# Performance work log

Measured on AMD Instinct MI355X. Metric: run time of the kernel, lower is better.

Reference implementation:

```python
import jax, jax.numpy as jnp
import numpy as np

D_MODEL = 512
NHEAD = 8
D_K = D_MODEL // NHEAD
SCALE = float(np.sqrt(D_K))


def setup_inputs() -> dict:
    key = jax.random.key(0)
    ks = jax.random.split(key, 11)
    B, S = 2, 4096
    std = 1.0 / np.sqrt(D_MODEL)
    inp = {
        'q': jax.random.normal(ks[0], (B, S, D_MODEL), jnp.float32),
        'k': jax.random.normal(ks[1], (B, S, D_MODEL), jnp.float32),
        'v': jax.random.normal(ks[2], (B, S, D_MODEL), jnp.float32),
        'w_q': jax.random.normal(ks[3], (D_MODEL, D_MODEL), jnp.float32) * std,
        'b_q': jax.random.normal(ks[4], (D_MODEL,), jnp.float32) * std,
        'w_k': jax.random.normal(ks[5], (D_MODEL, D_MODEL), jnp.float32) * std,
        'b_k': jax.random.normal(ks[6], (D_MODEL,), jnp.float32) * std,
        'w_v': jax.random.normal(ks[7], (D_MODEL, D_MODEL), jnp.float32) * std,
        'b_v': jax.random.normal(ks[8], (D_MODEL,), jnp.float32) * std,
        'w_o': jax.random.normal(ks[9], (D_MODEL, D_MODEL), jnp.float32) * std,
        'b_o': jax.random.normal(ks[10], (D_MODEL,), jnp.float32) * std,
    }
    return inp


def reference(q, k, v, w_q, b_q, w_k, b_k, w_v, b_v, w_o, b_o):
    B, S, _ = q.shape
    # torch Linear: y = x @ W.T + b
    def proj(x, W, b):
        y = x @ W.T + b
        return y.reshape(B, -1, NHEAD, D_K).transpose(0, 2, 1, 3)  # [B,H,S,Dk]
    qh = proj(q, w_q, b_q)
    kh = proj(k, w_k, b_k)
    vh = proj(v, w_v, b_v)
    scores = jnp.einsum('bhsd,bhtd->bhst', qh, kh) / SCALE  # [B,H,S,S]
    attn = jax.nn.softmax(scores, axis=-1)
    out = jnp.einsum('bhst,bhtd->bhsd', attn, vh)  # [B,H,S,Dk]
    out = out.transpose(0, 2, 1, 3).reshape(B, S, D_MODEL)
    return out @ w_o.T + b_o
```

## Files before the change

### kernel.cpp

```cpp
#include <hip/hip_runtime.h>
#include <stdint.h>

#define DM 512
#define S_LEN 4096
#define NH 8
#define DK 64

typedef __attribute__((ext_vector_type(8))) short bf16x8;
typedef __attribute__((ext_vector_type(4))) float f32x4;

#define QSCALE 0.18033688011112042f
#define NEGBIAS -17.312340490667562f

__device__ inline ushort f2bf(float f) {
  union { float f; uint32_t u; } v; v.f = f;
  uint32_t r = v.u + 0x7fff + ((v.u >> 16) & 1);
  return (ushort)(r >> 16);
}
__device__ inline uint32_t fu(float f) {
  union { float f; uint32_t u; } v; v.f = f; return v.u;
}
__device__ inline uint32_t pktrunc(float lo, float hi) {
  return __builtin_amdgcn_perm(fu(hi), fu(lo), 0x07060302);
}

__device__ inline void async_cp16(const ushort* g, ushort* l) {
  __builtin_amdgcn_global_load_lds((const __attribute__((address_space(1))) void*)g,
                                   (__attribute__((address_space(3))) void*)l, 16, 0, 0);
}

__global__ __launch_bounds__(256) void cvt_all(
    const float4* __restrict__ s0, ushort* __restrict__ d0,
    const float4* __restrict__ s1, ushort* __restrict__ d1,
    const float4* __restrict__ s2, ushort* __restrict__ d2,
    const float4* __restrict__ s3, ushort* __restrict__ d3,
    const float4* __restrict__ x0, ushort* __restrict__ y0,
    const float4* __restrict__ x1, ushort* __restrict__ y1,
    const float4* __restrict__ x2, ushort* __restrict__ y2) {
  if (blockIdx.x < 256) {
    int i = blockIdx.x * 256 + threadIdx.x;
    { float4 v = s0[i]; ushort4 o = {f2bf(v.x), f2bf(v.y), f2bf(v.z), f2bf(v.w)}; *(ushort4*)&d0[i * 4] = o; }
    { float4 v = s1[i]; ushort4 o = {f2bf(v.x), f2bf(v.y), f2bf(v.z), f2bf(v.w)}; *(ushort4*)&d1[i * 4] = o; }
    { float4 v = s2[i]; ushort4 o = {f2bf(v.x), f2bf(v.y), f2bf(v.z), f2bf(v.w)}; *(ushort4*)&d2[i * 4] = o; }
    { float4 v = s3[i]; ushort4 o = {f2bf(v.x), f2bf(v.y), f2bf(v.z), f2bf(v.w)}; *(ushort4*)&d3[i * 4] = o; }
  } else {
    int b = blockIdx.x - 256;
    #pragma unroll
    for (int r = 0; r < 2; r++) {
      int i = (b * 2 + r) * 256 + threadIdx.x;
      { float4 v = x0[i]; ushort4 o = {f2bf(v.x), f2bf(v.y), f2bf(v.z), f2bf(v.w)}; *(ushort4*)&y0[i * 4] = o; }
      { float4 v = x1[i]; ushort4 o = {f2bf(v.x), f2bf(v.y), f2bf(v.z), f2bf(v.w)}; *(ushort4*)&y1[i * 4] = o; }
      { float4 v = x2[i]; ushort4 o = {f2bf(v.x), f2bf(v.y), f2bf(v.z), f2bf(v.w)}; *(ushort4*)&y2[i * 4] = o; }
    }
  }
}

__global__ __launch_bounds__(256) void gemm_proj(
    const ushort* __restrict__ xq, const ushort* __restrict__ xk, const ushort* __restrict__ xv,
    const ushort* __restrict__ wq, const ushort* __restrict__ wk, const ushort* __restrict__ wv,
    const float* __restrict__ bq, const float* __restrict__ bk, const float* __restrict__ bv,
    ushort* __restrict__ Qh, ushort* __restrict__ Kh, ushort* __restrict__ VhT) {
  const ushort* A; const ushort* Bt; const float* bias; float cs;
  if (blockIdx.z == 0)      { A = xq; Bt = wq; bias = bq; cs = QSCALE; }
  else if (blockIdx.z == 1) { A = xk; Bt = wk; bias = bk; cs = 1.0f; }
  else                      { A = xv; Bt = wv; bias = bv; cs = 1.0f; }

  __shared__ ushort As[2][64 * 32];
  __shared__ ushort Bs[2][128 * 32];
  const int tid = threadIdx.x;
  const int w = tid >> 6, lane = tid & 63;
  const int quad = lane >> 4, l16 = lane & 15;
  const int wm = w >> 1, wn = w & 1;
  const int m0 = blockIdx.x * 64, n0 = blockIdx.y * 128;
  const f32x4 zero4 = {0.f, 0.f, 0.f, 0.f};

  f32x4 acc[2][4];
  #pragma unroll
  for (int i = 0; i < 2; i++)
    #pragma unroll
    for (int j = 0; j < 4; j++) acc[i][j] = zero4;

  #define PSTAGE(KB, BUF) do {                                                        \
    const int k0_ = (KB) * 32;                                                        \
    { int idx = tid;                                                \
      async_cp16(&A[(size_t)(m0 + (idx >> 2)) * DM + k0_ + (idx & 3) * 8], &As[BUF][idx * 8]); } \
    _Pragma("unroll")                                                                 \
    for (int r_ = 0; r_ < 2; r_++) {                                \
      int idx = r_ * 256 + tid;                                                       \
      async_cp16(&Bt[(size_t)(n0 + (idx >> 2)) * DM + k0_ + (idx & 3) * 8], &Bs[BUF][idx * 8]); \
    }                                                                                 \
  } while (0)

  PSTAGE(0, 0);
  __syncthreads();

  for (int kb = 0; kb < 16; kb++) {
    const int cur = kb & 1;
    if (kb < 15) PSTAGE(kb + 1, cur ^ 1);
    bf16x8 af[2], bfr[4];
    #pragma unroll
    for (int i = 0; i < 2; i++)
      af[i]  = *(const bf16x8*)&As[cur][(wm * 32 + i * 16 + l16) * 32 + quad * 8];
    #pragma unroll
    for (int j = 0; j < 4; j++)
      bfr[j] = *(const bf16x8*)&Bs[cur][(wn * 64 + j * 16 + l16) * 32 + quad * 8];
    #pragma unroll
    for (int i = 0; i < 2; i++)
      #pragma unroll
      for (int j = 0; j < 4; j++)
        acc[i][j] = __builtin_amdgcn_mfma_f32_16x16x32_bf16(af[i], bfr[j], acc[i][j], 0, 0, 0);
    __syncthreads();
  }

  if (blockIdx.z != 2) {
    ushort* C = (blockIdx.z == 0) ? Qh : Kh;
    #pragma unroll
    for (int j = 0; j < 4; j++) {
      int col_g = n0 + wn * 64 + j * 16 + l16;
      float bv = bias[col_g];
      int h = col_g >> 6, d = col_g & 63;
      #pragma unroll
      for (int i = 0; i < 2; i++) {
        #pragma unroll
        for (int r = 0; r < 4; r++) {
          int row_g = m0 + wm * 32 + i * 16 + quad * 4 + r;
          int b = row_g >> 12, s = row_g & 4095;
          C[(((size_t)(b * NH + h) << 12) + s) * DK + d] = f2bf((acc[i][j][r] + bv) * cs);
        }
      }
    }
  } else {
    #pragma unroll
    for (int j = 0; j < 4; j++) {
      int col_g = n0 + wn * 64 + j * 16 + l16;
      float bv = bias[col_g];
      int h = col_g >> 6, d = col_g & 63;
      #pragma unroll
      for (int i = 0; i < 2; i++) {
        int row0 = m0 + wm * 32 + i * 16 + quad * 4;
        int b = row0 >> 12, s0 = row0 & 4095;
        int sl = s0 & 31;
        int sp = (s0 & ~31) | (((sl >> 2) & 3) << 3) | (((sl >> 4) & 1) << 2);
        ushort4 pk = {f2bf(acc[i][j][0] + bv), f2bf(acc[i][j][1] + bv),
                      f2bf(acc[i][j][2] + bv), f2bf(acc[i][j][3] + bv)};
        *(ushort4*)&VhT[((size_t)(b * NH + h) * DK + d) * S_LEN + sp] = pk;
      }
    }
  }
}

__global__ __launch_bounds__(256) void gemm_out(const ushort* __restrict__ A,
                                                const ushort* __restrict__ Bt,
                                                const float* __restrict__ bias,
                                                float* __restrict__ C) {
  __shared__ ushort As[2][64 * 32];
  __shared__ ushort Bs[2][128 * 32];
  const int tid = threadIdx.x;
  const int w = tid >> 6, lane = tid & 63;
  const int quad = lane >> 4, l16 = lane & 15;
  const int wm = w >> 1, wn = w & 1;
  const int m0 = blockIdx.x * 64, n0 = blockIdx.y * 128;
  const f32x4 zero4 = {0.f, 0.f, 0.f, 0.f};

  f32x4 acc[2][4];
  #pragma unroll
  for (int i = 0; i < 2; i++)
    #pragma unroll
    for (int j = 0; j < 4; j++) acc[i][j] = zero4;

  #define OSTAGE(KB, BUF) do {                                                        \
    const int k0_ = (KB) * 32;                                                        \
    { int idx = tid;                                                                  \
      async_cp16(&A[(size_t)(m0 + (idx >> 2)) * DM + k0_ + (idx & 3) * 8], &As[BUF][idx * 8]); } \
    _Pragma("unroll")                                                                 \
    for (int r_ = 0; r_ < 2; r_++) {                                                  \
      int idx = r_ * 256 + tid;                                                       \
      async_cp16(&Bt[(size_t)(n0 + (idx >> 2)) * DM + k0_ + (idx & 3) * 8], &Bs[BUF][idx * 8]); \
    }                                                                                 \
  } while (0)

  OSTAGE(0, 0);
  __syncthreads();

  for (int kb = 0; kb < 16; kb++) {
    const int cur = kb & 1;
    if (kb < 15) OSTAGE(kb + 1, cur ^ 1);
    bf16x8 af[2], bfr[4];
    #pragma unroll
    for (int i = 0; i < 2; i++)
      af[i]  = *(const bf16x8*)&As[cur][(wm * 32 + i * 16 + l16) * 32 + quad * 8];
    #pragma unroll
    for (int j = 0; j < 4; j++)
      bfr[j] = *(const bf16x8*)&Bs[cur][(wn * 64 + j * 16 + l16) * 32 + quad * 8];
    #pragma unroll
    for (int i = 0; i < 2; i++)
      #pragma unroll
      for (int j = 0; j < 4; j++)
        acc[i][j] = __builtin_amdgcn_mfma_f32_16x16x32_bf16(af[i], bfr[j], acc[i][j], 0, 0, 0);
    __syncthreads();
  }

  #pragma unroll
  for (int j = 0; j < 4; j++) {
    int col_g = n0 + wn * 64 + j * 16 + l16;
    float bv = bias[col_g];
    #pragma unroll
    for (int i = 0; i < 2; i++) {
      #pragma unroll
      for (int r = 0; r < 4; r++) {
        int row_g = m0 + wm * 32 + i * 16 + quad * 4 + r;
        C[(size_t)row_g * DM + col_g] = acc[i][j][r] + bv;
      }
    }
  }
}

typedef union { bf16x8 v; uint32_t u[4]; } pfu;

__global__ __launch_bounds__(512, 4) void attn(const ushort* __restrict__ Qh,
                                               const ushort* __restrict__ Kh,
                                               const ushort* __restrict__ VhT,
                                               ushort* __restrict__ O) {
  __shared__ ushort smem[2][16384];
  const int tid = threadIdx.x;
  const int w = tid >> 6, lane = tid & 63;
  const int quad = lane >> 4, l16 = lane & 15;
  const int half = w >> 2;
  const int qw = w & 3;
  const int bh = blockIdx.x;
  const int q0 = blockIdx.y * 128 + qw * 32;
  const size_t base = (size_t)bh * S_LEN * DK;
  const f32x4 zero4 = {0.f, 0.f, 0.f, 0.f};
  const f32x4 negb = {NEGBIAS, NEGBIAS, NEGBIAS, NEGBIAS};
  const short one_bf = (short)0x3F80;
  const bf16x8 ones = {one_bf, one_bf, one_bf, one_bf, one_bf, one_bf, one_bf, one_bf};

  if (blockIdx.y >= 16) {
    #pragma unroll
    for (int i = 0; i < 6; i++) __builtin_amdgcn_s_sleep(7);
  }

  bf16x8 qf[2][2];
  #pragma unroll
  for (int i = 0; i < 2; i++)
    #pragma unroll
    for (int c = 0; c < 2; c++)
      qf[i][c] = *(const bf16x8*)&Qh[base + (size_t)(q0 + i * 16 + l16) * DK + c * 32 + quad * 8];

  f32x4 o[2][4];
  f32x4 l_acc[2];
  #pragma unroll
  for (int i = 0; i < 2; i++) {
    l_acc[i] = zero4;
    #pragma unroll
    for (int n = 0; n < 4; n++) o[i][n] = zero4;
  }

  #define STAGE(IT, BUF) do {                                                         \
    const int t0_ = (IT) * 128;                                                       \
    _Pragma("unroll")                                                                 \
    for (int r_ = 0; r_ < 2; r_++) {                                                  \
      int idx = r_ * 512 + tid;                                                       \
      int row = idx >> 3;                                                             \
      int cl = ((idx & 7) << 4) ^ ((row & 7) << 4);                                   \
      async_cp16(&Kh[base + (size_t)(t0_ + row) * DK + (cl >> 1)], &smem[BUF][idx * 8]); \
    }                                                                                 \
    _Pragma("unroll")                                                                 \
    for (int r_ = 0; r_ < 2; r_++) {                                                  \
      int idx = r_ * 512 + tid;                                                       \
      int row = idx >> 4;                                                             \
      int cl = ((idx & 15) << 4) ^ ((row & 7) << 4);                                  \
      async_cp16(&VhT[base + (size_t)row * S_LEN + t0_ + (cl >> 1)], &smem[BUF][8192 + idx * 8]); \
    }                                                                                 \
  } while (0)

  STAGE(0, 0);
  __syncthreads();

  const int swz = (l16 & 7) << 4;

  for (int it = 0; it < 32; it++) {
    const int cur = it & 1;
    if (it < 31) STAGE(it + 1, cur ^ 1);
    const ushort* Kb = &smem[cur][0];
    const ushort* Vb = &smem[cur][8192];

    bf16x8 kf[4][2];
    #pragma unroll
    for (int s = 0; s < 4; s++) {
      int row = half * 64 + s * 16 + l16;
      kf[s][0] = *(const bf16x8*)&Kb[row * 64 + ((( 0 + quad * 16) ^ swz) >> 1)];
      kf[s][1] = *(const bf16x8*)&Kb[row * 64 + (((64 + quad * 16) ^ swz) >> 1)];
    }
    f32x4 sc[2][4];
    __builtin_amdgcn_s_setprio(1);
    #pragma unroll
    for (int i = 0; i < 2; i++)
      #pragma unroll
      for (int s = 0; s < 4; s++) {
        f32x4 t = negb;
        t = __builtin_amdgcn_mfma_f32_16x16x32_bf16(kf[s][0], qf[i][0], t, 0, 0, 0);
        t = __builtin_amdgcn_mfma_f32_16x16x32_bf16(kf[s][1], qf[i][1], t, 0, 0, 0);
        sc[i][s] = t;
      }
    __builtin_amdgcn_s_setprio(0);
    float p[2][4][4];
    #pragma unroll
    for (int i = 0; i < 2; i++)
      #pragma unroll
      for (int s = 0; s < 4; s++)
        #pragma unroll
        for (int r = 0; r < 4; r++)
          p[i][s][r] = __builtin_amdgcn_exp2f(sc[i][s][r]);
    pfu pf[2][2];
    #pragma unroll
    for (int i = 0; i < 2; i++)
      #pragma unroll
      for (int ppl = 0; ppl < 2; ppl++) {
        int s0 = ppl * 2, s1 = ppl * 2 + 1;
        pf[i][ppl].u[0] = pktrunc(p[i][s0][0], p[i][s0][1]);
        pf[i][ppl].u[1] = pktrunc(p[i][s0][2], p[i][s0][3]);
        pf[i][ppl].u[2] = pktrunc(p[i][s1][0], p[i][s1][1]);
        pf[i][ppl].u[3] = pktrunc(p[i][s1][2], p[i][s1][3]);
        l_acc[i] = __builtin_amdgcn_mfma_f32_16x16x32_bf16(pf[i][ppl].v, ones, l_acc[i], 0, 0, 0);
      }
    bf16x8 vf[4][2];
    #pragma unroll
    for (int n = 0; n < 4; n++) {
      int row = n * 16 + l16;
      #pragma unroll
      for (int ppl = 0; ppl < 2; ppl++)
        vf[n][ppl] = *(const bf16x8*)&Vb[row * 128 + ((((half * 2 + ppl) * 64 + quad * 16) ^ swz) >> 1)];
    }
    __builtin_amdgcn_s_setprio(1);
    #pragma unroll
    for (int n = 0; n < 4; n++)
      #pragma unroll
      for (int ppl = 0; ppl < 2; ppl++)
        #pragma unroll
        for (int i = 0; i < 2; i++)
          o[i][n] = __builtin_amdgcn_mfma_f32_16x16x32_bf16(pf[i][ppl].v, vf[n][ppl], o[i][n], 0, 0, 0);
    __builtin_amdgcn_s_setprio(0);

    __syncthreads();
  }

  float* red = (float*)smem;
  const int roff = (qw * 64 + lane) * 40;
  if (half == 1) {
    #pragma unroll
    for (int i = 0; i < 2; i++) {
      #pragma unroll
      for (int n = 0; n < 4; n++)
        *(f32x4*)&red[roff + (i * 4 + n) * 4] = o[i][n];
      *(f32x4*)&red[roff + 32 + i * 4] = l_acc[i];
    }
  }
  __syncthreads();
  if (half == 0) {
    #pragma unroll
    for (int i = 0; i < 2; i++) {
      #pragma unroll
      for (int n = 0; n < 4; n++)
        o[i][n] += *(const f32x4*)&red[roff + (i * 4 + n) * 4];
      l_acc[i] += *(const f32x4*)&red[roff + 32 + i * 4];
    }
    const int b = bh >> 3, h = bh & 7;
    #pragma unroll
    for (int i = 0; i < 2; i++) {
      #pragma unroll
      for (int r = 0; r < 4; r++) {
        float inv = 1.0f / l_acc[i][r];
        int qq = q0 + i * 16 + quad * 4 + r;
        #pragma unroll
        for (int n = 0; n < 4; n++) {
          int d = n * 16 + l16;
          O[(size_t)(b * S_LEN + qq) * DM + h * DK + d] = f2bf(o[i][n][r] * inv);
        }
      }
    }
  }
}

extern "C" void kernel_launch(void* const* d_in, const int* in_sizes, int n_in,
                              void* d_out, int out_size, void* d_ws, size_t ws_size,
                              hipStream_t stream) {
  const float* q   = (const float*)d_in[0];
  const float* k   = (const float*)d_in[1];
  const float* v   = (const float*)d_in[2];
  const float* w_q = (const float*)d_in[3];
  const float* b_q = (const float*)d_in[4];
  const float* w_k = (const float*)d_in[5];
  const float* b_k = (const float*)d_in[6];
  const float* w_v = (const float*)d_in[7];
  const float* b_v = (const float*)d_in[8];
  const float* w_o = (const float*)d_in[9];
  const float* b_o = (const float*)d_in[10];

  const size_t W_ELEMS = (size_t)DM * DM;
  const size_t X_ELEMS = (size_t)2 * S_LEN * DM;
  const size_t HEADS_ELEMS = (size_t)2 * NH * S_LEN * DK;
  ushort* wqb = (ushort*)d_ws;
  ushort* wkb = wqb + W_ELEMS;
  ushort* wvb = wkb + W_ELEMS;
  ushort* wob = wvb + W_ELEMS;
  ushort* Xq  = wob + W_ELEMS;
  ushort* Xk  = Xq + X_ELEMS;
  ushort* Xv  = Xk + X_ELEMS;
  ushort* Qh  = Xv + X_ELEMS;
  ushort* Kh  = Qh + HEADS_ELEMS;
  ushort* VhT = Kh + HEADS_ELEMS;
  ushort* AttO = VhT + HEADS_ELEMS;

  cvt_all<<<2304, 256, 0, stream>>>((const float4*)w_q, wqb, (const float4*)w_k, wkb,
                                    (const float4*)w_v, wvb, (const float4*)w_o, wob,
                                    (const float4*)q, Xq, (const float4*)k, Xk,
                                    (const float4*)v, Xv);
  gemm_proj<<<dim3(128, 4, 3), 256, 0, stream>>>(Xq, Xk, Xv, wqb, wkb, wvb,
                                                 b_q, b_k, b_v, Qh, Kh, VhT);
  attn<<<dim3(16, 32), 512, 0, stream>>>(Qh, Kh, VhT, AttO);
  gemm_out<<<dim3(128, 4), 256, 0, stream>>>(AttO, wob, b_o, (float*)d_out);
}
```

Measured before the change: 212.7 us.

## Fuse activation fp32-to-bf16 conversion into projection GEMM staging

Drops the separate conversion pass over the q/k/v activations. The projection GEMM now async-copies fp32 activation tiles straight into LDS and converts them to bf16 by truncation while building MFMA fragments. LDS layouts for both GEMMs are also reorganised into k-chunk-major order so each lane's fragment read is contiguous and less bank-conflicted. In exchange, the projection kernel reads twice as many activation bytes per tile, uses more LDS, and rounds by truncation instead of round-to-nearest.

```diff
diff --git a/kernel.cpp b/kernel.cpp
--- a/kernel.cpp
+++ b/kernel.cpp
@@ -24,49 +24,34 @@
   return __builtin_amdgcn_perm(fu(hi), fu(lo), 0x07060302);
 }
 
-__device__ inline void async_cp16(const ushort* g, ushort* l) {
+__device__ inline void async_cp16(const void* g, void* l) {
   __builtin_amdgcn_global_load_lds((const __attribute__((address_space(1))) void*)g,
                                    (__attribute__((address_space(3))) void*)l, 16, 0, 0);
 }
 
-__global__ __launch_bounds__(256) void cvt_all(
-    const float4* __restrict__ s0, ushort* __restrict__ d0,
-    const float4* __restrict__ s1, ushort* __restrict__ d1,
-    const float4* __restrict__ s2, ushort* __restrict__ d2,
-    const float4* __restrict__ s3, ushort* __restrict__ d3,
-    const float4* __restrict__ x0, ushort* __restrict__ y0,
-    const float4* __restrict__ x1, ushort* __restrict__ y1,
-    const float4* __restrict__ x2, ushort* __restrict__ y2) {
-  if (blockIdx.x < 256) {
-    int i = blockIdx.x * 256 + threadIdx.x;
-    { float4 v = s0[i]; ushort4 o = {f2bf(v.x), f2bf(v.y), f2bf(v.z), f2bf(v.w)}; *(ushort4*)&d0[i * 4] = o; }
-    { float4 v = s1[i]; ushort4 o = {f2bf(v.x), f2bf(v.y), f2bf(v.z), f2bf(v.w)}; *(ushort4*)&d1[i * 4] = o; }
-    { float4 v = s2[i]; ushort4 o = {f2bf(v.x), f2bf(v.y), f2bf(v.z), f2bf(v.w)}; *(ushort4*)&d2[i * 4] = o; }
-    { float4 v = s3[i]; ushort4 o = {f2bf(v.x), f2bf(v.y), f2bf(v.z), f2bf(v.w)}; *(ushort4*)&d3[i * 4] = o; }
-  } else {
-    int b = blockIdx.x - 256;
-    #pragma unroll
-    for (int r = 0; r < 2; r++) {
-      int i = (b * 2 + r) * 256 + threadIdx.x;
-      { float4 v = x0[i]; ushort4 o = {f2bf(v.x), f2bf(v.y), f2bf(v.z), f2bf(v.w)}; *(ushort4*)&y0[i * 4] = o; }
-      { float4 v = x1[i]; ushort4 o = {f2bf(v.x), f2bf(v.y), f2bf(v.z), f2bf(v.w)}; *(ushort4*)&y1[i * 4] = o; }
-      { float4 v = x2[i]; ushort4 o = {f2bf(v.x), f2bf(v.y), f2bf(v.z), f2bf(v.w)}; *(ushort4*)&y2[i * 4] = o; }
-    }
-  }
+__global__ __launch_bounds__(256) void cvt_w(const float4* __restrict__ s0, ushort* __restrict__ d0,
+                                             const float4* __restrict__ s1, ushort* __restrict__ d1,
+                                             const float4* __restrict__ s2, ushort* __restrict__ d2,
+                                             const float4* __restrict__ s3, ushort* __restrict__ d3) {
+  int i = blockIdx.x * 256 + threadIdx.x;
+  { float4 v = s0[i]; ushort4 o = {f2bf(v.x), f2bf(v.y), f2bf(v.z), f2bf(v.w)}; *(ushort4*)&d0[i * 4] = o; }
+  { float4 v = s1[i]; ushort4 o = {f2bf(v.x), f2bf(v.y), f2bf(v.z), f2bf(v.w)}; *(ushort4*)&d1[i * 4] = o; }
+  { float4 v = s2[i]; ushort4 o = {f2bf(v.x), f2bf(v.y), f2bf(v.z), f2bf(v.w)}; *(ushort4*)&d2[i * 4] = o; }
+  { float4 v = s3[i]; ushort4 o = {f2bf(v.x), f2bf(v.y), f2bf(v.z), f2bf(v.w)}; *(ushort4*)&d3[i * 4] = o; }
 }
 
 __global__ __launch_bounds__(256) void gemm_proj(
-    const ushort* __restrict__ xq, const ushort* __restrict__ xk, const ushort* __restrict__ xv,
+    const float* __restrict__ q, const float* __restrict__ k, const float* __restrict__ v,
     const ushort* __restrict__ wq, const ushort* __restrict__ wk, const ushort* __restrict__ wv,
     const float* __restrict__ bq, const float* __restrict__ bk, const float* __restrict__ bv,
     ushort* __restrict__ Qh, ushort* __restrict__ Kh, ushort* __restrict__ VhT) {
-  const ushort* A; const ushort* Bt; const float* bias; float cs;
-  if (blockIdx.z == 0)      { A = xq; Bt = wq; bias = bq; cs = QSCALE; }
-  else if (blockIdx.z == 1) { A = xk; Bt = wk; bias = bk; cs = 1.0f; }
-  else                      { A = xv; Bt = wv; bias = bv; cs = 1.0f; }
-
-  __shared__ ushort As[2][64 * 32];
-  __shared__ ushort Bs[2][128 * 32];
+  const float* A; const ushort* Bt; const float* bias; float cs;
+  if (blockIdx.z == 0)      { A = q; Bt = wq; bias = bq; cs = QSCALE; }
+  else if (blockIdx.z == 1) { A = k; Bt = wk; bias = bk; cs = 1.0f; }
+  else                      { A = v; Bt = wv; bias = bv; cs = 1.0f; }
+
+  __shared__ float  Asf[2][2048];
+  __shared__ ushort Bsp[2][4096];
   const int tid = threadIdx.x;
   const int w = tid >> 6, lane = tid & 63;
   const int quad = lane >> 4, l16 = lane & 15;
@@ -82,12 +67,17 @@
 
   #define PSTAGE(KB, BUF) do {                                                        \
     const int k0_ = (KB) * 32;                                                        \
-    { int idx = tid;                                                \
-      async_cp16(&A[(size_t)(m0 + (idx >> 2)) * DM + k0_ + (idx & 3) * 8], &As[BUF][idx * 8]); } \
     _Pragma("unroll")                                                                 \
-    for (int r_ = 0; r_ < 2; r_++) {                                \
+    for (int r_ = 0; r_ < 2; r_++) {                       \
       int idx = r_ * 256 + tid;                                                       \
-      async_cp16(&Bt[(size_t)(n0 + (idx >> 2)) * DM + k0_ + (idx & 3) * 8], &Bs[BUF][idx * 8]); \
+      int c = idx >> 6, row = idx & 63;                                               \
+      async_cp16(&A[(size_t)(m0 + row) * DM + k0_ + c * 4], &Asf[BUF][idx * 4]);      \
+    }                                                                                 \
+    _Pragma("unroll")                                                                 \
+    for (int r_ = 0; r_ < 2; r_++) {                       \
+      int idx = r_ * 256 + tid;                                                       \
+      int c = idx >> 7, row = idx & 127;                                              \
+      async_cp16(&Bt[(size_t)(n0 + row) * DM + k0_ + c * 8], &Bsp[BUF][idx * 8]);     \
     }                                                                                 \
   } while (0)
 
@@ -99,11 +89,18 @@
     if (kb < 15) PSTAGE(kb + 1, cur ^ 1);
     bf16x8 af[2], bfr[4];
     #pragma unroll
-    for (int i = 0; i < 2; i++)
-      af[i]  = *(const bf16x8*)&As[cur][(wm * 32 + i * 16 + l16) * 32 + quad * 8];
+    for (int i = 0; i < 2; i++) {
+      int r = wm * 32 + i * 16 + l16;
+      f32x4 a0 = *(const f32x4*)&Asf[cur][((quad * 2 + 0) * 64 + r) * 4];
+      f32x4 a1 = *(const f32x4*)&Asf[cur][((quad * 2 + 1) * 64 + r) * 4];
+      union { bf16x8 v; uint32_t u[4]; } t;
+      t.u[0] = pktrunc(a0.x, a0.y); t.u[1] = pktrunc(a0.z, a0.w);
+      t.u[2] = pktrunc(a1.x, a1.y); t.u[3] = pktrunc(a1.z, a1.w);
+      af[i] = t.v;
+    }
     #pragma unroll
     for (int j = 0; j < 4; j++)
-      bfr[j] = *(const bf16x8*)&Bs[cur][(wn * 64 + j * 16 + l16) * 32 + quad * 8];
+      bfr[j] = *(const bf16x8*)&Bsp[cur][(quad * 128 + wn * 64 + j * 16 + l16) * 8];
     #pragma unroll
     for (int i = 0; i < 2; i++)
       #pragma unroll
@@ -153,8 +150,8 @@
                                                 const ushort* __restrict__ Bt,
                                                 const float* __restrict__ bias,
                                                 float* __restrict__ C) {
-  __shared__ ushort As[2][64 * 32];
-  __shared__ ushort Bs[2][128 * 32];
+  __shared__ ushort Asp[2][2048];
+  __shared__ ushort Bsp[2][4096];
   const int tid = threadIdx.x;
   const int w = tid >> 6, lane = tid & 63;
   const int quad = lane >> 4, l16 = lane & 15;
@@ -170,12 +167,14 @@
 
   #define OSTAGE(KB, BUF) do {                                                        \
     const int k0_ = (KB) * 32;                                                        \
-    { int idx = tid;                                                                  \
-      async_cp16(&A[(size_t)(m0 + (idx >> 2)) * DM + k0_ + (idx & 3) * 8], &As[BUF][idx * 8]); } \
+    { int idx = tid;                                                \
+      int c = idx >> 6, row = idx & 63;                                               \
+      async_cp16(&A[(size_t)(m0 + row) * DM + k0_ + c * 8], &Asp[BUF][idx * 8]); }    \
     _Pragma("unroll")                                                                 \
-    for (int r_ = 0; r_ < 2; r_++) {                                                  \
+    for (int r_ = 0; r_ < 2; r_++) {                                \
       int idx = r_ * 256 + tid;                                                       \
-      async_cp16(&Bt[(size_t)(n0 + (idx >> 2)) * DM + k0_ + (idx & 3) * 8], &Bs[BUF][idx * 8]); \
+      int c = idx >> 7, row = idx & 127;                                              \
+      async_cp16(&Bt[(size_t)(n0 + row) * DM + k0_ + c * 8], &Bsp[BUF][idx * 8]);     \
     }                                                                                 \
   } while (0)
 
@@ -188,10 +187,10 @@
     bf16x8 af[2], bfr[4];
     #pragma unroll
     for (int i = 0; i < 2; i++)
-      af[i]  = *(const bf16x8*)&As[cur][(wm * 32 + i * 16 + l16) * 32 + quad * 8];
+      af[i]  = *(const bf16x8*)&Asp[cur][(quad * 64 + wm * 32 + i * 16 + l16) * 8];
     #pragma unroll
     for (int j = 0; j < 4; j++)
-      bfr[j] = *(const bf16x8*)&Bs[cur][(wn * 64 + j * 16 + l16) * 32 + quad * 8];
+      bfr[j] = *(const bf16x8*)&Bsp[cur][(quad * 128 + wn * 64 + j * 16 + l16) * 8];
     #pragma unroll
     for (int i = 0; i < 2; i++)
       #pragma unroll
@@ -398,25 +397,19 @@
   const float* b_o = (const float*)d_in[10];
 
   const size_t W_ELEMS = (size_t)DM * DM;
-  const size_t X_ELEMS = (size_t)2 * S_LEN * DM;
   const size_t HEADS_ELEMS = (size_t)2 * NH * S_LEN * DK;
   ushort* wqb = (ushort*)d_ws;
   ushort* wkb = wqb + W_ELEMS;
   ushort* wvb = wkb + W_ELEMS;
   ushort* wob = wvb + W_ELEMS;
-  ushort* Xq  = wob + W_ELEMS;
-  ushort* Xk  = Xq + X_ELEMS;
-  ushort* Xv  = Xk + X_ELEMS;
-  ushort* Qh  = Xv + X_ELEMS;
+  ushort* Qh  = wob + W_ELEMS;
   ushort* Kh  = Qh + HEADS_ELEMS;
   ushort* VhT = Kh + HEADS_ELEMS;
   ushort* AttO = VhT + HEADS_ELEMS;
 
-  cvt_all<<<2304, 256, 0, stream>>>((const float4*)w_q, wqb, (const float4*)w_k, wkb,
-                                    (const float4*)w_v, wvb, (const float4*)w_o, wob,
-                                    (const float4*)q, Xq, (const float4*)k, Xk,
-                                    (const float4*)v, Xv);
-  gemm_proj<<<dim3(128, 4, 3), 256, 0, stream>>>(Xq, Xk, Xv, wqb, wkb, wvb,
+  cvt_w<<<256, 256, 0, stream>>>((const float4*)w_q, wqb, (const float4*)w_k, wkb,
+                                 (const float4*)w_v, wvb, (const float4*)w_o, wob);
+  gemm_proj<<<dim3(128, 4, 3), 256, 0, stream>>>(q, k, v, wqb, wkb, wvb,
                                                  b_q, b_k, b_v, Qh, Kh, VhT);
   attn<<<dim3(16, 32), 512, 0, stream>>>(Qh, Kh, VhT, AttO);
   gemm_out<<<dim3(128, 4), 256, 0, stream>>>(AttO, wob, b_o, (float*)d_out);
```

Result: slower. 245.4 us (+15.4%).

## Triple-buffer projection GEMMs with explicit vmcnt waits and k-chunk-major LDS layout

Applied to the files above, without the earlier changes.

Both projection GEMM kernels move from a double-buffered LDS pipeline to a three-stage ring that prefetches two k-blocks ahead. A single barrier per iteration is gated by an explicit s_waitcnt vmcnt, replacing the two __syncthreads per step. The LDS tile layout changes from row-major 32-wide rows to k-chunk-major 8-element slabs, so each quad's 16-byte fragment reads fall in contiguous, bank-friendly addresses. This costs 50% more LDS per block, which may reduce occupancy, and relies on hand-counted vmcnt values that must match the number of async loads per stage.

```diff
diff --git a/kernel.cpp b/kernel.cpp
--- a/kernel.cpp
+++ b/kernel.cpp
@@ -24,7 +24,7 @@
   return __builtin_amdgcn_perm(fu(hi), fu(lo), 0x07060302);
 }
 
-__device__ inline void async_cp16(const ushort* g, ushort* l) {
+__device__ inline void async_cp16(const void* g, void* l) {
   __builtin_amdgcn_global_load_lds((const __attribute__((address_space(1))) void*)g,
                                    (__attribute__((address_space(3))) void*)l, 16, 0, 0);
 }
@@ -65,8 +65,8 @@
   else if (blockIdx.z == 1) { A = xk; Bt = wk; bias = bk; cs = 1.0f; }
   else                      { A = xv; Bt = wv; bias = bv; cs = 1.0f; }
 
-  __shared__ ushort As[2][64 * 32];
-  __shared__ ushort Bs[2][128 * 32];
+  __shared__ ushort Asp[3][2048];
+  __shared__ ushort Bsp[3][4096];
   const int tid = threadIdx.x;
   const int w = tid >> 6, lane = tid & 63;
   const int quad = lane >> 4, l16 = lane & 15;
@@ -82,34 +82,42 @@
 
   #define PSTAGE(KB, BUF) do {                                                        \
     const int k0_ = (KB) * 32;                                                        \
+    ushort* asp_ = &Asp[BUF][0];                                                      \
+    ushort* bsp_ = &Bsp[BUF][0];                                                      \
     { int idx = tid;                                                \
-      async_cp16(&A[(size_t)(m0 + (idx >> 2)) * DM + k0_ + (idx & 3) * 8], &As[BUF][idx * 8]); } \
+      int c = idx >> 6, row = idx & 63;                                               \
+      async_cp16(&A[(size_t)(m0 + row) * DM + k0_ + c * 8], &asp_[idx * 8]); }        \
     _Pragma("unroll")                                                                 \
     for (int r_ = 0; r_ < 2; r_++) {                                \
       int idx = r_ * 256 + tid;                                                       \
-      async_cp16(&Bt[(size_t)(n0 + (idx >> 2)) * DM + k0_ + (idx & 3) * 8], &Bs[BUF][idx * 8]); \
+      int c = idx >> 7, row = idx & 127;                                              \
+      async_cp16(&Bt[(size_t)(n0 + row) * DM + k0_ + c * 8], &bsp_[idx * 8]);         \
     }                                                                                 \
   } while (0)
 
   PSTAGE(0, 0);
-  __syncthreads();
-
+  PSTAGE(1, 1);
+
+  #pragma unroll
   for (int kb = 0; kb < 16; kb++) {
-    const int cur = kb & 1;
-    if (kb < 15) PSTAGE(kb + 1, cur ^ 1);
+    if (kb < 15) asm volatile("s_waitcnt vmcnt(3)" ::: "memory");
+    else         asm volatile("s_waitcnt vmcnt(0)" ::: "memory");
+    __builtin_amdgcn_s_barrier();
+    __builtin_amdgcn_sched_barrier(0);
+    if (kb < 14) PSTAGE(kb + 2, (kb + 2) % 3);
+    const int cur = kb % 3;
     bf16x8 af[2], bfr[4];
     #pragma unroll
     for (int i = 0; i < 2; i++)
-      af[i]  = *(const bf16x8*)&As[cur][(wm * 32 + i * 16 + l16) * 32 + quad * 8];
+      af[i]  = *(const bf16x8*)&Asp[cur][(quad * 64 + wm * 32 + i * 16 + l16) * 8];
     #pragma unroll
     for (int j = 0; j < 4; j++)
-      bfr[j] = *(const bf16x8*)&Bs[cur][(wn * 64 + j * 16 + l16) * 32 + quad * 8];
+      bfr[j] = *(const bf16x8*)&Bsp[cur][(quad * 128 + wn * 64 + j * 16 + l16) * 8];
     #pragma unroll
     for (int i = 0; i < 2; i++)
       #pragma unroll
       for (int j = 0; j < 4; j++)
         acc[i][j] = __builtin_amdgcn_mfma_f32_16x16x32_bf16(af[i], bfr[j], acc[i][j], 0, 0, 0);
-    __syncthreads();
   }
 
   if (blockIdx.z != 2) {
@@ -153,8 +161,8 @@
                                                 const ushort* __restrict__ Bt,
                                                 const float* __restrict__ bias,
                                                 float* __restrict__ C) {
-  __shared__ ushort As[2][64 * 32];
-  __shared__ ushort Bs[2][128 * 32];
+  __shared__ ushort Asp[3][2048];
+  __shared__ ushort Bsp[3][4096];
   const int tid = threadIdx.x;
   const int w = tid >> 6, lane = tid & 63;
   const int quad = lane >> 4, l16 = lane & 15;
@@ -170,34 +178,42 @@
 
   #define OSTAGE(KB, BUF) do {                                                        \
     const int k0_ = (KB) * 32;                                                        \
-    { int idx = tid;                                                                  \
-      async_cp16(&A[(size_t)(m0 + (idx >> 2)) * DM + k0_ + (idx & 3) * 8], &As[BUF][idx * 8]); } \
+    ushort* asp_ = &Asp[BUF][0];                                                      \
+    ushort* bsp_ = &Bsp[BUF][0];                                                      \
+    { int idx = tid;                                                \
+      int c = idx >> 6, row = idx & 63;                                               \
+      async_cp16(&A[(size_t)(m0 + row) * DM + k0_ + c * 8], &asp_[idx * 8]); }        \
     _Pragma("unroll")                                                                 \
-    for (int r_ = 0; r_ < 2; r_++) {                                                  \
+    for (int r_ = 0; r_ < 2; r_++) {                                \
       int idx = r_ * 256 + tid;                                                       \
-      async_cp16(&Bt[(size_t)(n0 + (idx >> 2)) * DM + k0_ + (idx & 3) * 8], &Bs[BUF][idx * 8]); \
+      int c = idx >> 7, row = idx & 127;                                              \
+      async_cp16(&Bt[(size_t)(n0 + row) * DM + k0_ + c * 8], &bsp_[idx * 8]);         \
     }                                                                                 \
   } while (0)
 
   OSTAGE(0, 0);
-  __syncthreads();
-
+  OSTAGE(1, 1);
+
+  #pragma unroll
   for (int kb = 0; kb < 16; kb++) {
-    const int cur = kb & 1;
-    if (kb < 15) OSTAGE(kb + 1, cur ^ 1);
+    if (kb < 15) asm volatile("s_waitcnt vmcnt(3)" ::: "memory");
+    else         asm volatile("s_waitcnt vmcnt(0)" ::: "memory");
+    __builtin_amdgcn_s_barrier();
+    __builtin_amdgcn_sched_barrier(0);
+    if (kb < 14) OSTAGE(kb + 2, (kb + 2) % 3);
+    const int cur = kb % 3;
     bf16x8 af[2], bfr[4];
     #pragma unroll
     for (int i = 0; i < 2; i++)
-      af[i]  = *(const bf16x8*)&As[cur][(wm * 32 + i * 16 + l16) * 32 + quad * 8];
+      af[i]  = *(const bf16x8*)&Asp[cur][(quad * 64 + wm * 32 + i * 16 + l16) * 8];
     #pragma unroll
     for (int j = 0; j < 4; j++)
-      bfr[j] = *(const bf16x8*)&Bs[cur][(wn * 64 + j * 16 + l16) * 32 + quad * 8];
+      bfr[j] = *(const bf16x8*)&Bsp[cur][(quad * 128 + wn * 64 + j * 16 + l16) * 8];
     #pragma unroll
     for (int i = 0; i < 2; i++)
       #pragma unroll
       for (int j = 0; j < 4; j++)
         acc[i][j] = __builtin_amdgcn_mfma_f32_16x16x32_bf16(af[i], bfr[j], acc[i][j], 0, 0, 0);
-    __syncthreads();
   }
 
   #pragma unroll
```

Result: slower. 230.3 us (+8.3%).
